# Kernel tuning notes

Measured on AMD Instinct MI355X. Metric: run time of the kernel, lower is better.

Reference implementation:

```python
import jax, jax.numpy as jnp
import numpy as np

B, N, K_NN, H, IN_DIM, OUT_DIM = 32, 1024, 16, 64, 4, 2
START = 2 * H   # EdgeConv MLP input width (cat[x_i, x_j - x_i])
MID = 3 * H // 2


def _elu(x):
    return jax.nn.elu(x)


def _lin_init(key, fan_in, fan_out):
    k1, k2 = jax.random.split(key)
    lim = 1.0 / np.sqrt(fan_in)
    W = jax.random.uniform(k1, (fan_in, fan_out), minval=-lim, maxval=lim, dtype=jnp.float32)
    b = jax.random.uniform(k2, (fan_out,), minval=-lim, maxval=lim, dtype=jnp.float32)
    return W, b


def setup_inputs():
    key = jax.random.key(0)
    ks = jax.random.split(key, 11)
    inp = {
        "x": jax.random.normal(ks[0], (B, N, IN_DIM), dtype=jnp.float32),
        "norm": jnp.array([1e-3, 1e-1, 1.0 / 3.15, 1.0 / 3000.0], dtype=jnp.float32),
    }
    dims = [("in1", IN_DIM, H // 2), ("in2", H // 2, H), ("in3", H, H),
            ("c1a", START, MID), ("c1b", MID, H),
            ("c2a", START, MID), ("c2b", MID, H),
            ("o1", H, H), ("o2", H, H // 2), ("o3", H // 2, OUT_DIM)]
    for i, (nm, fi, fo) in enumerate(dims):
        W, b = _lin_init(ks[i + 1], fi, fo)
        inp[nm + "_W"] = W
        inp[nm + "_b"] = b
    return inp


def _pdist2(x):
    # squared pairwise distances per graph: [B,n,n]
    x2 = jnp.sum(x * x, -1)
    d2 = x2[:, :, None] + x2[:, None, :] - 2.0 * jnp.einsum('bnh,bmh->bnm', x, x)
    return jnp.maximum(d2, 0.0)


def _knn(x, valid, k):
    # knn_graph(loop=False) restricted to valid (non-padded) target columns
    b, n, _ = x.shape
    d2 = _pdist2(jax.lax.stop_gradient(x))
    bad = jnp.eye(n, dtype=bool)[None] | (~valid)[:, None, :]
    d2 = jnp.where(bad, jnp.inf, d2)
    _, idx = jax.lax.top_k(-d2, k)                      # [B,n,k] neighbor ids
    bi = jnp.arange(b)[:, None, None]
    ni = jnp.arange(n)[None, :, None]
    Kd = jnp.zeros((b, n, n), bool).at[bi, ni, idx].set(True)   # dense kNN adjacency
    return idx, Kd


def _edge_mlp(e, W1, b1, W2, b2):
    return _elu(_elu(e @ W1 + b1) @ W2 + b2)


def _edgeconv(x, valid, idx, Kd, W1, b1, W2, b2):
    # EdgeConv(aggr='add') over to_undirected(knn_graph): message nn([x_i, x_j - x_i])
    b, n, h = x.shape
    xj = jax.vmap(lambda xg, ig: xg[ig])(x, idx)        # [B,n,k,h] gathered neighbors
    xi = jnp.broadcast_to(x[:, :, None, :], xj.shape)
    agg = _edge_mlp(jnp.concatenate([xi, xj - xi], -1), W1, b1, W2, b2).sum(2)
    # reverse edges added by to_undirected; coalesce drops duplicates of mutual kNN pairs
    mutual = jnp.take_along_axis(jnp.swapaxes(Kd, 1, 2), idx, axis=2)  # [B,n,k]
    w_rev = ((~mutual) & valid[:, :, None]).astype(x.dtype)
    msg_rev = _edge_mlp(jnp.concatenate([xj, xi - xj], -1), W1, b1, W2, b2) * w_rev[..., None]
    seg = (jnp.arange(b)[:, None, None] * n + idx).reshape(-1)
    agg_rev = jax.ops.segment_sum(msg_rev.reshape(-1, h), seg, num_segments=b * n).reshape(b, n, h)
    return agg + agg_rev


def _norm_cut_w(x, A):
    # normalized_cut_2d: ||x_i - x_j|| * (1/deg_i + 1/deg_j) on edges, -inf elsewhere
    dist = jnp.sqrt(_pdist2(x))
    invdeg = 1.0 / A.sum(-1).astype(x.dtype)
    cut = dist * (invdeg[:, :, None] + invdeg[:, None, :])
    return jnp.where(A, cut, -jnp.inf)


def _graclus(Wm):
    # greedy heavy-edge matching (deterministic node order), like graclus
    n = Wm.shape[-1]

    def match_one(Wg):
        def body(i, st):
            unmatched, cluster = st
            wi = jnp.where(unmatched, Wg[i], -jnp.inf)
            j = jnp.argmax(wi)
            ok = unmatched[i] & jnp.isfinite(wi[j])
            r = jnp.minimum(i, j)
            cluster = jnp.where(ok, cluster.at[i].set(r).at[j].set(r), cluster)
            unmatched = unmatched.at[i].set(False)
            unmatched = jnp.where(ok, unmatched.at[j].set(False), unmatched)
            return unmatched, cluster

        return jax.lax.fori_loop(0, n, body, (jnp.ones(n, bool), jnp.arange(n)))[1]

    return jax.vmap(match_one)(jax.lax.stop_gradient(Wm))


def _max_pool(x, cluster):
    # max over each cluster; representative = min node index; padded slots masked
    b, n, h = x.shape
    pooled = jax.vmap(lambda xg, cg: jax.ops.segment_max(xg, cg, num_segments=n))(x, cluster)
    counts = jax.vmap(lambda cg: jnp.zeros(n, jnp.int32).at[cg].add(1))(cluster)
    valid = counts > 0
    return jnp.where(valid[..., None], pooled, 0.0), valid


def _forward(x, norm, in1_W, in1_b, in2_W, in2_b, in3_W, in3_b,
             c1a_W, c1a_b, c1b_W, c1b_b, c2a_W, c2a_b, c2b_W, c2b_b,
             o1_W, o1_b, o2_W, o2_b, o3_W, o3_b):
    h0 = x * norm
    h0 = _elu(_elu(_elu(h0 @ in1_W + in1_b) @ in2_W + in2_b) @ in3_W + in3_b)
    valid0 = jnp.ones(h0.shape[:2], bool)
    idx1, K1 = _knn(h0, valid0, K_NN)
    h1 = _edgeconv(h0, valid0, idx1, K1, c1a_W, c1a_b, c1b_W, c1b_b)
    A1 = K1 | jnp.swapaxes(K1, 1, 2)
    cl = _graclus(_norm_cut_w(jax.lax.stop_gradient(h1), A1))
    h1p, valid1 = _max_pool(h1, cl)
    idx2, K2 = _knn(h1p, valid1, K_NN)
    h2 = _edgeconv(h1p, valid1, idx2, K2, c2a_W, c2a_b, c2b_W, c2b_b)
    # 2nd graclus max_pool_x followed by global_max_pool == global max over valid nodes
    g = jnp.max(jnp.where(valid1[..., None], h2, -jnp.inf), axis=1)   # [B,H]
    return _elu(_elu(g @ o1_W + o1_b) @ o2_W + o2_b) @ o3_W + o3_b


def reference(x, norm, in1_W, in1_b, in2_W, in2_b, in3_W, in3_b,
              c1a_W, c1a_b, c1b_W, c1b_b, c2a_W, c2a_b, c2b_W, c2b_b,
              o1_W, o1_b, o2_W, o2_b, o3_W, o3_b):
    return _forward(x, norm, in1_W, in1_b, in2_W, in2_b, in3_W, in3_b,
                    c1a_W, c1a_b, c1b_W, c1b_b, c2a_W, c2a_b, c2b_W, c2b_b,
                    o1_W, o1_b, o2_W, o2_b, o3_W, o3_b)
```

## Files before the change

### kernel.cpp

```cpp
#include <hip/hip_runtime.h>
#include <cmath>


#define DEVI __device__ __forceinline__
constexpr int B_   = 32;
constexpr int N_   = 1024;
constexpr int NN   = B_ * N_;
constexpr int NCH  = 8;
constexpr int CHW  = 128;
constexpr int ECAP = 128;

#define INFF (__builtin_huge_valf())

DEVI float elu_(float x)  { return x > 0.f ? x : expm1f(x); }
DEVI float eluf(float x)  { return x > 0.f ? x : __expf(x) - 1.f; }

__global__ __launch_bounds__(256) void k_input(
    const float* __restrict__ x, const float* __restrict__ nrm,
    const float* __restrict__ w1, const float* __restrict__ b1,
    const float* __restrict__ w2, const float* __restrict__ b2,
    const float* __restrict__ w3, const float* __restrict__ b3,
    float* __restrict__ h0, float* __restrict__ x2a)
{
  __shared__ float s1[128], sb1[32], s2[2048], sb2[64], s3[4096], sb3[64];
  int tid = threadIdx.x;
  for (int t = tid; t < 128; t += 256) s1[t] = w1[t];
  if (tid < 32) sb1[tid] = b1[tid];
  for (int t = tid; t < 2048; t += 256) s2[t] = w2[t];
  if (tid < 64) sb2[tid] = b2[tid];
  for (int t = tid; t < 4096; t += 256) s3[t] = w3[t];
  if (tid < 64) sb3[tid] = b3[tid];
  __syncthreads();
  int n = blockIdx.x * 256 + tid;
  float xi[4];
#pragma unroll
  for (int d = 0; d < 4; d++) xi[d] = x[n * 4 + d] * nrm[d];
  float a1[32];
#pragma unroll
  for (int c = 0; c < 32; c++) {
    float a = sb1[c];
#pragma unroll
    for (int d = 0; d < 4; d++) a += xi[d] * s1[d * 32 + c];
    a1[c] = elu_(a);
  }
  float a2[64];
#pragma unroll
  for (int c = 0; c < 64; c++) {
    float a = sb2[c];
#pragma unroll
    for (int d = 0; d < 32; d++) a += a1[d] * s2[d * 64 + c];
    a2[c] = elu_(a);
  }
  float ss = 0.f;
#pragma unroll
  for (int c = 0; c < 64; c++) {
    float a = sb3[c];
#pragma unroll
    for (int d = 0; d < 64; d++) a += a2[d] * s3[d * 64 + c];
    a = elu_(a);
    h0[n * 64 + c] = a;
    ss += a * a;
  }
  x2a[n] = ss;
}

__global__ __launch_bounds__(256) void k_knn(
    const float4* __restrict__ X4, const float* __restrict__ X2,
    const unsigned* __restrict__ vbits, const int* __restrict__ vrows,
    float* __restrict__ pd, unsigned short* __restrict__ pix)
{
  __shared__ float xs[CHW * 64];
  __shared__ float xs2[CHW];
  __shared__ unsigned vm[32];
  int bid = blockIdx.x;
  int swz = (bid & 7) * 128 + (bid >> 3);
  int b  = swz >> 5;
  int rt = (swz >> 3) & 3;
  int ch = swz & 7;
  int tid = threadIdx.x;
  int j0 = ch * CHW;
  for (int t = tid; t < CHW * 16; t += 256) {
    int r = t >> 4, q = t & 15;
    float4 v = X4[(b * N_ + j0 + r) * 16 + q];
    *reinterpret_cast<float4*>(&xs[r * 64 + q * 4]) = v;
  }
  for (int t = tid; t < CHW; t += 256) xs2[t] = X2[b * N_ + j0 + t];
  for (int t = tid; t < 32; t += 256) vm[t] = vbits ? vbits[b * 32 + t] : 0xFFFFFFFFu;
  __syncthreads();
  int i = rt * 256 + tid;
  int gi = b * N_ + i;
  if (vrows && !vrows[gi]) return;
  float4 xi4[16];
#pragma unroll
  for (int q = 0; q < 16; q++) xi4[q] = X4[gi * 16 + q];
  float x2i = X2[gi];
  float topd[16]; int topi[16];
#pragma unroll
  for (int q = 0; q < 16; q++) { topd[q] = INFF; topi[q] = 0xFFFF; }
  for (int jj = 0; jj < CHW; ++jj) {
    int j = j0 + jj;
    if (j == i) continue;
    if (!((vm[j >> 5] >> (j & 31)) & 1u)) continue;
    const float4* xr = reinterpret_cast<const float4*>(&xs[jj * 64]);
    float dot = 0.f;
#pragma unroll
    for (int q = 0; q < 16; q++) {
      float4 v = xr[q];
      dot += xi4[q].x * v.x + xi4[q].y * v.y + xi4[q].z * v.z + xi4[q].w * v.w;
    }
    float d2 = fmaxf(x2i + xs2[jj] - 2.f * dot, 0.f);
    if (d2 < topd[15]) {
      topd[15] = d2; topi[15] = j;
#pragma unroll
      for (int p = 15; p > 0; --p) {
        if (topd[p] < topd[p - 1]) {
          float td = topd[p]; topd[p] = topd[p - 1]; topd[p - 1] = td;
          int   ti = topi[p]; topi[p] = topi[p - 1]; topi[p - 1] = ti;
        }
      }
    }
  }
  size_t base = ((size_t)gi * NCH + ch) * 16;
#pragma unroll
  for (int q = 0; q < 16; q++) { pd[base + q] = topd[q]; pix[base + q] = (unsigned short)topi[q]; }
}

__global__ __launch_bounds__(64) void k_merge(
    const float* __restrict__ pd, const unsigned short* __restrict__ pix,
    const int* __restrict__ vrows,
    unsigned* __restrict__ Kb, unsigned* __restrict__ KTb)
{
  __shared__ unsigned lbm[64][33];
  int tid = threadIdx.x;
  int gi = blockIdx.x * 64 + tid;
  int b = gi >> 10, i = gi & 1023;
  if (vrows && !vrows[gi]) return;
#pragma unroll
  for (int w = 0; w < 32; w++) lbm[tid][w] = 0u;
  float topd[16]; int topi[16];
#pragma unroll
  for (int q = 0; q < 16; q++) { topd[q] = INFF; topi[q] = 0; }
  for (int s = 0; s < NCH; ++s) {
    size_t base = ((size_t)gi * NCH + s) * 16;
#pragma unroll 1
    for (int q = 0; q < 16; q++) {
      float d = pd[base + q];
      if (!(d < topd[15])) break;
      topd[15] = d; topi[15] = pix[base + q];
#pragma unroll
      for (int p = 15; p > 0; --p) {
        if (topd[p] < topd[p - 1]) {
          float td = topd[p]; topd[p] = topd[p - 1]; topd[p - 1] = td;
          int   ti = topi[p]; topi[p] = topi[p - 1]; topi[p - 1] = ti;
        }
      }
    }
  }
#pragma unroll
  for (int q = 0; q < 16; q++) {
    int j = topi[q];
    lbm[tid][j >> 5] |= (1u << (j & 31));
    atomicOr(&KTb[((size_t)b * N_ + j) * 32 + (i >> 5)], 1u << (i & 31));
  }
#pragma unroll
  for (int w = 0; w < 32; w++) Kb[(size_t)gi * 32 + w] = lbm[tid][w];
}

__global__ __launch_bounds__(256) void k_elist(
    const unsigned* __restrict__ Kb, const unsigned* __restrict__ KTb,
    unsigned short* __restrict__ E, int* __restrict__ ecnt, float* __restrict__ invdeg)
{
  int gi = blockIdx.x * 256 + threadIdx.x;
  unsigned short* e = E + (size_t)gi * ECAP;
  int n = 0;
  for (int w = 0; w < 32; w++) {
    unsigned m = Kb[(size_t)gi * 32 + w] | KTb[(size_t)gi * 32 + w];
    while (m) {
      int bit = __ffs(m) - 1; m &= m - 1;
      if (n < ECAP) e[n] = (unsigned short)(w * 32 + bit);
      n++;
    }
  }
  ecnt[gi] = n < ECAP ? n : ECAP;
  if (invdeg) invdeg[gi] = 1.f / (float)n;
}

__global__ __launch_bounds__(256) void k_uv(
    const float* __restrict__ X, const float* __restrict__ W1, const float* __restrict__ b1,
    float* __restrict__ wb, float* __restrict__ vb)
{
  __shared__ float wc[64 * 96], wv[64 * 96];
  int tid = threadIdx.x;
  for (int t = tid; t < 64 * 96; t += 256) {
    int d = t / 96, c = t - d * 96;
    float hv = W1[(d + 64) * 96 + c];
    wv[t] = hv;
    wc[t] = W1[d * 96 + c] - hv;
  }
  __syncthreads();
  int n = blockIdx.x * 256 + tid;
  float xi[64];
#pragma unroll
  for (int q = 0; q < 16; q++) {
    float4 v = reinterpret_cast<const float4*>(X)[n * 16 + q];
    xi[q * 4] = v.x; xi[q * 4 + 1] = v.y; xi[q * 4 + 2] = v.z; xi[q * 4 + 3] = v.w;
  }
#pragma unroll 1
  for (int c4 = 0; c4 < 24; c4++) {
    float aw0 = b1[c4 * 4 + 0], aw1 = b1[c4 * 4 + 1], aw2 = b1[c4 * 4 + 2], aw3 = b1[c4 * 4 + 3];
    float av0 = 0.f, av1 = 0.f, av2 = 0.f, av3 = 0.f;
#pragma unroll
    for (int d = 0; d < 64; d++) {
      float4 c = *reinterpret_cast<const float4*>(&wc[d * 96 + c4 * 4]);
      float4 v = *reinterpret_cast<const float4*>(&wv[d * 96 + c4 * 4]);
      float xd = xi[d];
      aw0 += xd * c.x; aw1 += xd * c.y; aw2 += xd * c.z; aw3 += xd * c.w;
      av0 += xd * v.x; av1 += xd * v.y; av2 += xd * v.z; av3 += xd * v.w;
    }
    wb[(size_t)n * 96 + c4 * 4 + 0] = aw0; wb[(size_t)n * 96 + c4 * 4 + 1] = aw1;
    wb[(size_t)n * 96 + c4 * 4 + 2] = aw2; wb[(size_t)n * 96 + c4 * 4 + 3] = aw3;
    vb[(size_t)n * 96 + c4 * 4 + 0] = av0; vb[(size_t)n * 96 + c4 * 4 + 1] = av1;
    vb[(size_t)n * 96 + c4 * 4 + 2] = av2; vb[(size_t)n * 96 + c4 * 4 + 3] = av3;
  }
}

__global__ __launch_bounds__(256) void k_conv(
    const float* __restrict__ wbuf, const float* __restrict__ vbuf,
    const unsigned short* __restrict__ E, const int* __restrict__ ecnt,
    const int* __restrict__ vrows,
    const float* __restrict__ W2, const float* __restrict__ b2,
    float* __restrict__ out, float* __restrict__ x2out)
{
  __shared__ float w2s[96 * 64];
  __shared__ float b2s[64];
  __shared__ float wds[64 * 100];
  int tid = threadIdx.x;
  int bid = blockIdx.x;
  int swz = (bid & 7) * 64 + (bid >> 3);
  int dst0 = swz * 64;
  for (int t = tid; t < 96 * 64; t += 256) w2s[t] = W2[t];
  if (tid < 64) b2s[tid] = b2[tid];
  for (int t = tid; t < 64 * 96; t += 256) {
    int l = t / 96, c = t - l * 96;
    wds[l * 100 + c] = wbuf[(size_t)(dst0 + l) * 96 + c];
  }
  __syncthreads();
  int dl = tid >> 2, p = tid & 3;
  int dst = dst0 + dl;
  if (vrows && !vrows[dst]) return;
  int cnt = ecnt[dst];
  const unsigned short* e = E + (size_t)dst * ECAP;
  int gb = dst & ~(N_ - 1);
  float agg[16];
#pragma unroll
  for (int o = 0; o < 16; o++) agg[o] = 0.f;

#pragma unroll 1
  for (int k = 0; k < cnt; k += 2) {
    bool hasB = (k + 1 < cnt);
    int sA = gb + e[k];
    int sB = hasB ? gb + e[k + 1] : sA;
    const float4* vA = reinterpret_cast<const float4*>(vbuf + (size_t)sA * 96);
    const float4* vB = reinterpret_cast<const float4*>(vbuf + (size_t)sB * 96);
    float sa[16], sb_[16];
#pragma unroll
    for (int o = 0; o < 16; o++) { sa[o] = b2s[p * 16 + o]; sb_[o] = sa[o]; }
#pragma unroll 1
    for (int c4 = 0; c4 < 24; c4++) {
      float4 wv = *reinterpret_cast<const float4*>(&wds[dl * 100 + c4 * 4]);
      float4 a4 = vA[c4];
      float4 b4 = vB[c4];
      float tA0 = eluf(wv.x + a4.x), tA1 = eluf(wv.y + a4.y),
            tA2 = eluf(wv.z + a4.z), tA3 = eluf(wv.w + a4.w);
      float tB0 = eluf(wv.x + b4.x), tB1 = eluf(wv.y + b4.y),
            tB2 = eluf(wv.z + b4.z), tB3 = eluf(wv.w + b4.w);
      const float* wr = &w2s[(c4 * 4) * 64 + p * 16];
#pragma unroll
      for (int o4 = 0; o4 < 4; o4++) {
        float4 w0 = *reinterpret_cast<const float4*>(wr + 0 * 64 + o4 * 4);
        float4 w1 = *reinterpret_cast<const float4*>(wr + 1 * 64 + o4 * 4);
        float4 w2 = *reinterpret_cast<const float4*>(wr + 2 * 64 + o4 * 4);
        float4 w3 = *reinterpret_cast<const float4*>(wr + 3 * 64 + o4 * 4);
        sa [o4*4+0] += tA0*w0.x + tA1*w1.x + tA2*w2.x + tA3*w3.x;
        sa [o4*4+1] += tA0*w0.y + tA1*w1.y + tA2*w2.y + tA3*w3.y;
        sa [o4*4+2] += tA0*w0.z + tA1*w1.z + tA2*w2.z + tA3*w3.z;
        sa [o4*4+3] += tA0*w0.w + tA1*w1.w + tA2*w2.w + tA3*w3.w;
        sb_[o4*4+0] += tB0*w0.x + tB1*w1.x + tB2*w2.x + tB3*w3.x;
        sb_[o4*4+1] += tB0*w0.y + tB1*w1.y + tB2*w2.y + tB3*w3.y;
        sb_[o4*4+2] += tB0*w0.z + tB1*w1.z + tB2*w2.z + tB3*w3.z;
        sb_[o4*4+3] += tB0*w0.w + tB1*w1.w + tB2*w2.w + tB3*w3.w;
      }
    }
#pragma unroll
    for (int o = 0; o < 16; o++) agg[o] += eluf(sa[o]);
    if (hasB) {
#pragma unroll
      for (int o = 0; o < 16; o++) agg[o] += eluf(sb_[o]);
    }
  }
  float4* o4p = reinterpret_cast<float4*>(out + (size_t)dst * 64 + p * 16);
#pragma unroll
  for (int q = 0; q < 4; q++)
    o4p[q] = make_float4(agg[q*4], agg[q*4+1], agg[q*4+2], agg[q*4+3]);
  if (x2out) {
    float s = 0.f;
#pragma unroll
    for (int o = 0; o < 16; o++) s += agg[o] * agg[o];
    s += __shfl_xor(s, 1, 64);
    s += __shfl_xor(s, 2, 64);
    if (p == 0) x2out[dst] = s;
  }
}

__global__ __launch_bounds__(256) void k_wgt(
    const float* __restrict__ h1, const float* __restrict__ x2h,
    const float* __restrict__ invdeg, const unsigned short* __restrict__ E,
    const int* __restrict__ ecnt, unsigned* __restrict__ cw)
{
  int bid = blockIdx.x;
  int swz = (bid & 7) * 16 + (bid >> 3);
  int gi = swz * 256 + threadIdx.x;
  int base = gi & ~(N_ - 1);
  float xi[64];
#pragma unroll
  for (int q = 0; q < 16; q++) {
    float4 v = reinterpret_cast<const float4*>(h1)[gi * 16 + q];
    xi[q * 4] = v.x; xi[q * 4 + 1] = v.y; xi[q * 4 + 2] = v.z; xi[q * 4 + 3] = v.w;
  }
  float x2i = x2h[gi];
  float idi = invdeg[gi];
  int cnt = ecnt[gi];
  const unsigned short* e = E + (size_t)gi * ECAP;
  unsigned* crow = cw + (size_t)gi * ECAP;
#pragma unroll 1
  for (int n = 0; n < cnt; n++) {
    int j = base + e[n];
    const float4* r = reinterpret_cast<const float4*>(h1 + (size_t)j * 64);
    float dot = 0.f;
#pragma unroll
    for (int q = 0; q < 16; q++) {
      float4 v = r[q];
      dot += xi[q * 4] * v.x + xi[q * 4 + 1] * v.y + xi[q * 4 + 2] * v.z + xi[q * 4 + 3] * v.w;
    }
    float d2 = fmaxf(x2i + x2h[j] - 2.f * dot, 0.f);
    float wgt = sqrtf(d2) * (idi + invdeg[j]);
    crow[n] = __float_as_uint(wgt);
  }
}

__global__ __launch_bounds__(256) void k_sort(
    const unsigned* __restrict__ cw, const unsigned short* __restrict__ E0,
    const int* __restrict__ ecnt, unsigned short* __restrict__ E)
{
  int node = (blockIdx.x * 256 + threadIdx.x) >> 6;
  int lane = threadIdx.x & 63;
  int cnt = ecnt[node];
  size_t rb = (size_t)node * ECAP;
  unsigned long long a = 0ull, b = 0ull;
  if (lane < cnt)
    a = ((unsigned long long)cw[rb + lane] << 32) | (unsigned)(~(unsigned)E0[rb + lane]);
  if (lane + 64 < cnt)
    b = ((unsigned long long)cw[rb + 64 + lane] << 32) | (unsigned)(~(unsigned)E0[rb + 64 + lane]);
#pragma unroll
  for (int k = 2; k <= 128; k <<= 1) {
#pragma unroll
    for (int jj = k >> 1; jj > 0; jj >>= 1) {
      if (jj == 64) {
        unsigned long long mx = a > b ? a : b;
        b = a > b ? b : a;
        a = mx;
      } else {
        unsigned long long oa = __shfl_xor(a, jj, 64);
        bool low   = (lane & jj) == 0;
        bool descA = (lane & k) == 0;
        a = ((low == descA) == (a > oa)) ? a : oa;
        unsigned long long ob = __shfl_xor(b, jj, 64);
        bool descB = (((lane + 64) & k) == 0);
        b = ((low == descB) == (b > ob)) ? b : ob;
      }
    }
  }
  E[rb + lane]      = (unsigned short)(~(unsigned)a);
  E[rb + 64 + lane] = (unsigned short)(~(unsigned)b);
}

__global__ __launch_bounds__(64) void k_graclus(
    const unsigned short* __restrict__ E,
    int* __restrict__ cluster, int* __restrict__ partner)
{
  int b = blockIdx.x, lane = threadIdx.x;
  int g0 = b * N_;
  const unsigned short* Eg = E + (size_t)g0 * ECAP;
  for (int t = lane; t < N_; t += 64) { cluster[g0 + t] = t; partner[g0 + t] = -1; }
  unsigned m16 = 0xFFFFu;
  unsigned long long below = (1ull << lane) - 1ull;

  unsigned short eA0, eA1, eB0, eB1, eC0, eC1, eD0, eD1;
#define LOADROW(E0v, E1v, row)                                                  \
  { size_t rb_ = (size_t)(row) * ECAP;                                          \
    E0v = Eg[rb_ + lane];                                                       \
    E1v = Eg[rb_ + 64 + lane]; }
  LOADROW(eA0, eA1, 0)
  LOADROW(eB0, eB1, 1)
  LOADROW(eC0, eC1, 2)
  LOADROW(eD0, eD1, 3)

  auto step = [&](int i, unsigned short e0, unsigned short e1) {
    unsigned mi = (unsigned)__builtin_amdgcn_readlane((int)m16, i >> 4);
    if ((mi >> (i & 15)) & 1u) {
      bool v0 = e0 != 0xFFFFu, v1 = e1 != 0xFFFFu;
      int j0 = e0 & (N_ - 1), j1 = e1 & (N_ - 1);
      unsigned gm0 = (unsigned)__shfl((int)m16, j0 >> 4, 64);
      unsigned gm1 = (unsigned)__shfl((int)m16, j1 >> 4, 64);
      bool p0 = v0 && ((gm0 >> (j0 & 15)) & 1u);
      bool p1 = v1 && ((gm1 >> (j1 & 15)) & 1u);
      unsigned long long m0 = __ballot(p0);
      unsigned long long m1 = __ballot(p1);
      unsigned long long mm = m0 ? m0 : m1;
      if (mm) {
        int sw = __ffsll((long long)mm) - 1;
        int jw = m0 ? __builtin_amdgcn_readlane(j0, sw)
                    : __builtin_amdgcn_readlane(j1, sw);
        unsigned clr = (lane == (jw >> 4)) ? (1u << (jw & 15)) : 0u;
        m16 &= ~clr;
        if (lane == 0) {
          int r = i < jw ? i : jw;
          int o = i ^ jw ^ r;
          cluster[g0 + o] = r;
          partner[g0 + r] = o;
        }
      }
      unsigned clri = (lane == (i >> 4)) ? (1u << (i & 15)) : 0u;
      m16 &= ~clri;
    }
  };

  for (int i = 0; i < N_; i += 4) {
    step(i, eA0, eA1);
    if (i + 4 < N_) LOADROW(eA0, eA1, i + 4)
    step(i + 1, eB0, eB1);
    if (i + 5 < N_) LOADROW(eB0, eB1, i + 5)
    step(i + 2, eC0, eC1);
    if (i + 6 < N_) LOADROW(eC0, eC1, i + 6)
    step(i + 3, eD0, eD1);
    if (i + 7 < N_) LOADROW(eD0, eD1, i + 7)
  }
#undef LOADROW
}

__global__ __launch_bounds__(256) void k_maxpool(
    const float* __restrict__ h1, const int* __restrict__ cluster, const int* __restrict__ partner,
    float* __restrict__ h1p, float* __restrict__ x2p, int* __restrict__ valid1,
    unsigned* __restrict__ vbits)
{
  int gi = blockIdx.x * 256 + threadIdx.x;
  int b = gi >> 10, i = gi & 1023;
  if (cluster[gi] == i) {
    int p = partner[gi];
    float s = 0.f;
#pragma unroll
    for (int q = 0; q < 16; q++) {
      float4 a = reinterpret_cast<const float4*>(h1)[gi * 16 + q];
      if (p >= 0) {
        float4 c = reinterpret_cast<const float4*>(h1)[(b * N_ + p) * 16 + q];
        a.x = fmaxf(a.x, c.x); a.y = fmaxf(a.y, c.y); a.z = fmaxf(a.z, c.z); a.w = fmaxf(a.w, c.w);
      }
      reinterpret_cast<float4*>(h1p)[gi * 16 + q] = a;
      s += a.x * a.x + a.y * a.y + a.z * a.z + a.w * a.w;
    }
    x2p[gi] = s; valid1[gi] = 1;
    atomicOr(&vbits[b * 32 + (i >> 5)], 1u << (i & 31));
  } else {
    float4 z = make_float4(0.f, 0.f, 0.f, 0.f);
#pragma unroll
    for (int q = 0; q < 16; q++) reinterpret_cast<float4*>(h1p)[gi * 16 + q] = z;
    x2p[gi] = 0.f; valid1[gi] = 0;
  }
}

__global__ __launch_bounds__(256) void k_final(
    const float* __restrict__ h2, const int* __restrict__ valid1,
    const float* __restrict__ o1W, const float* __restrict__ o1b,
    const float* __restrict__ o2W, const float* __restrict__ o2b,
    const float* __restrict__ o3W, const float* __restrict__ o3b,
    float* __restrict__ out)
{
  __shared__ float gm[4][64], g[64], l1[64], l2[32];
  int b = blockIdx.x, tid = threadIdx.x;
  int d = tid & 63, r = tid >> 6;
  float m = -INFF;
  for (int i = r; i < N_; i += 4) {
    if (valid1[b * N_ + i]) m = fmaxf(m, h2[(size_t)(b * N_ + i) * 64 + d]);
  }
  gm[r][d] = m;
  __syncthreads();
  if (tid < 64) g[d] = fmaxf(fmaxf(gm[0][d], gm[1][d]), fmaxf(gm[2][d], gm[3][d]));
  __syncthreads();
  if (tid < 64) {
    float a = o1b[tid];
    for (int c = 0; c < 64; c++) a += g[c] * o1W[c * 64 + tid];
    l1[tid] = elu_(a);
  }
  __syncthreads();
  if (tid < 32) {
    float a2 = o2b[tid];
    for (int c = 0; c < 64; c++) a2 += l1[c] * o2W[c * 32 + tid];
    l2[tid] = elu_(a2);
  }
  __syncthreads();
  if (tid < 2) {
    float a3 = o3b[tid];
    for (int c = 0; c < 32; c++) a3 += l2[c] * o3W[c * 2 + tid];
    out[b * 2 + tid] = a3;
  }
}

extern "C" void kernel_launch(void* const* d_in, const int* in_sizes, int n_in,
                              void* d_out, int out_size, void* d_ws, size_t ws_size,
                              hipStream_t stream)
{
  const float* x    = (const float*)d_in[0];
  const float* nrm  = (const float*)d_in[1];
  const float* in1W = (const float*)d_in[2];  const float* in1b = (const float*)d_in[3];
  const float* in2W = (const float*)d_in[4];  const float* in2b = (const float*)d_in[5];
  const float* in3W = (const float*)d_in[6];  const float* in3b = (const float*)d_in[7];
  const float* c1aW = (const float*)d_in[8];  const float* c1ab = (const float*)d_in[9];
  const float* c1bW = (const float*)d_in[10]; const float* c1bb = (const float*)d_in[11];
  const float* c2aW = (const float*)d_in[12]; const float* c2ab = (const float*)d_in[13];
  const float* c2bW = (const float*)d_in[14]; const float* c2bb = (const float*)d_in[15];
  const float* o1W  = (const float*)d_in[16]; const float* o1b  = (const float*)d_in[17];
  const float* o2W  = (const float*)d_in[18]; const float* o2b  = (const float*)d_in[19];
  const float* o3W  = (const float*)d_in[20]; const float* o3b  = (const float*)d_in[21];

  constexpr size_t O_H0    = 0;
  constexpr size_t O_X2A   = O_H0    + (size_t)NN * 64 * 4;
  constexpr size_t O_U     = O_X2A   + (size_t)NN * 4;
  constexpr size_t O_K     = O_U     + (size_t)NN * NCH * 16 * 6;
  constexpr size_t O_KT    = O_K     + (size_t)NN * 32 * 4;
  constexpr size_t O_H1    = O_KT    + (size_t)NN * 32 * 4;
  constexpr size_t O_X2H   = O_H1    + (size_t)NN * 64 * 4;
  constexpr size_t O_IDG   = O_X2H   + (size_t)NN * 4;
  constexpr size_t O_ECNT  = O_IDG   + (size_t)NN * 4;
  constexpr size_t O_CLU   = O_ECNT  + (size_t)NN * 4;
  constexpr size_t O_PAR   = O_CLU   + (size_t)NN * 4;
  constexpr size_t O_VAL   = O_PAR   + (size_t)NN * 4;
  constexpr size_t O_VBITS = O_VAL   + (size_t)NN * 4;
  constexpr size_t O_E     = O_VBITS + (size_t)B_ * 32 * 4;
  constexpr size_t TOTAL   = O_E     + (size_t)NN * ECAP * 2;
  if (ws_size < TOTAL) return;

  char* w = (char*)d_ws;
  float*          h0   = (float*)(w + O_H0);
  float*          x2a  = (float*)(w + O_X2A);
  float*          pdp  = (float*)(w + O_U);
  unsigned short* pip  = (unsigned short*)(w + O_U + (size_t)NN * NCH * 16 * 4);
  float*          wb   = (float*)(w + O_U);
  float*          vb   = (float*)(w + O_U + (size_t)NN * 96 * 4);
  unsigned*       cwt  = (unsigned*)(w + O_U);
  unsigned*       Kb   = (unsigned*)(w + O_K);
  unsigned*       KTb  = (unsigned*)(w + O_KT);
  float*          h1   = (float*)(w + O_H1);
  float*          x2h  = (float*)(w + O_X2H);
  float*          idg  = (float*)(w + O_IDG);
  int*            ecnt = (int*)(w + O_ECNT);
  int*            clu  = (int*)(w + O_CLU);
  int*            par  = (int*)(w + O_PAR);
  int*            val  = (int*)(w + O_VAL);
  unsigned*       vbits= (unsigned*)(w + O_VBITS);
  unsigned short* E    = (unsigned short*)(w + O_E);
  float* h1p = h0;
  float* x2p = x2a;
  float* h2  = h1;

  k_input<<<NN / 256, 256, 0, stream>>>(x, nrm, in1W, in1b, in2W, in2b, in3W, in3b, h0, x2a);
  k_knn<<<B_ * 32, 256, 0, stream>>>((const float4*)h0, x2a, nullptr, nullptr, pdp, pip);
  hipMemsetAsync(KTb, 0, (size_t)NN * 32 * 4, stream);
  k_merge<<<NN / 64, 64, 0, stream>>>(pdp, pip, nullptr, Kb, KTb);
  k_elist<<<NN / 256, 256, 0, stream>>>(Kb, KTb, E, ecnt, idg);
  k_uv<<<NN / 256, 256, 0, stream>>>(h0, c1aW, c1ab, wb, vb);
  k_conv<<<NN / 64, 256, 0, stream>>>(wb, vb, E, ecnt, nullptr, c1bW, c1bb, h1, x2h);
  k_wgt<<<NN / 256, 256, 0, stream>>>(h1, x2h, idg, E, ecnt, cwt);
  k_sort<<<NN / 4, 256, 0, stream>>>(cwt, E, ecnt, E);
  k_graclus<<<B_, 64, 0, stream>>>(E, clu, par);
  hipMemsetAsync(vbits, 0, (size_t)B_ * 32 * 4, stream);
  k_maxpool<<<NN / 256, 256, 0, stream>>>(h1, clu, par, h1p, x2p, val, vbits);
  k_knn<<<B_ * 32, 256, 0, stream>>>((const float4*)h1p, x2p, vbits, val, pdp, pip);
  hipMemsetAsync(Kb, 0, (size_t)NN * 32 * 4 * 2, stream);
  k_merge<<<NN / 64, 64, 0, stream>>>(pdp, pip, val, Kb, KTb);
  k_elist<<<NN / 256, 256, 0, stream>>>(Kb, KTb, E, ecnt, nullptr);
  k_uv<<<NN / 256, 256, 0, stream>>>(h1p, c2aW, c2ab, wb, vb);
  k_conv<<<NN / 64, 256, 0, stream>>>(wb, vb, E, ecnt, val, c2bW, c2bb, h2, nullptr);
  k_final<<<B_, 256, 0, stream>>>(h2, val, o1W, o1b, o2W, o2b, o3W, o3b, (float*)d_out);
}
```

Before: 1.750 ms.

## Sort EdgeConv destination nodes by degree to balance wavefront work

Adds a per-graph counting-sort kernel that orders nodes by edge count. k_conv then processes destinations through this permutation, so each wavefront handles nodes with similar neighbor-loop trip counts. Each block takes four interleaved degree buckets (low, high, and mirrored) to even out work across blocks. It also drops the early return for invalid rows, since these now cluster in zero-degree groups, and unrolls the inner channel loop by 4. The cost is an extra small kernel launch per conv and gathered, non-contiguous loads of wbuf rows.

```diff
diff --git a/kernel.cpp b/kernel.cpp
--- a/kernel.cpp
+++ b/kernel.cpp
@@ -185,6 +185,28 @@
   if (invdeg) invdeg[gi] = 1.f / (float)n;
 }
 
+__global__ __launch_bounds__(256) void k_perm(
+    const int* __restrict__ ecnt, unsigned short* __restrict__ perm)
+{
+  __shared__ int hist[ECAP + 1];
+  __shared__ int pfx[ECAP + 1];
+  int b = blockIdx.x, tid = threadIdx.x;
+  int g0 = b * N_;
+  for (int t = tid; t <= ECAP; t += 256) hist[t] = 0;
+  __syncthreads();
+  for (int t = tid; t < N_; t += 256) atomicAdd(&hist[ecnt[g0 + t]], 1);
+  __syncthreads();
+  if (tid == 0) {
+    int s = 0;
+    for (int d = 0; d <= ECAP; d++) { pfx[d] = s; s += hist[d]; }
+  }
+  __syncthreads();
+  for (int t = tid; t < N_; t += 256) {
+    int r = atomicAdd(&pfx[ecnt[g0 + t]], 1);
+    perm[g0 + r] = (unsigned short)t;
+  }
+}
+
 __global__ __launch_bounds__(256) void k_uv(
     const float* __restrict__ X, const float* __restrict__ W1, const float* __restrict__ b1,
     float* __restrict__ wb, float* __restrict__ vb)
@@ -227,30 +249,36 @@
 __global__ __launch_bounds__(256) void k_conv(
     const float* __restrict__ wbuf, const float* __restrict__ vbuf,
     const unsigned short* __restrict__ E, const int* __restrict__ ecnt,
-    const int* __restrict__ vrows,
+    const unsigned short* __restrict__ perm,
     const float* __restrict__ W2, const float* __restrict__ b2,
     float* __restrict__ out, float* __restrict__ x2out)
 {
   __shared__ float w2s[96 * 64];
   __shared__ float b2s[64];
   __shared__ float wds[64 * 100];
+  __shared__ unsigned short dstl[64];
   int tid = threadIdx.x;
   int bid = blockIdx.x;
   int swz = (bid & 7) * 64 + (bid >> 3);
-  int dst0 = swz * 64;
+  int g  = swz >> 4, kk = swz & 15;
+  int gb = g * N_;
   for (int t = tid; t < 96 * 64; t += 256) w2s[t] = W2[t];
   if (tid < 64) b2s[tid] = b2[tid];
+  if (tid < 64) {
+    int w = tid >> 4, r = tid & 15;
+    int wg = (w == 0) ? kk : (w == 1) ? 31 - kk : (w == 2) ? 32 + kk : 63 - kk;
+    dstl[tid] = perm[gb + wg * 16 + r];
+  }
+  __syncthreads();
   for (int t = tid; t < 64 * 96; t += 256) {
     int l = t / 96, c = t - l * 96;
-    wds[l * 100 + c] = wbuf[(size_t)(dst0 + l) * 96 + c];
+    wds[l * 100 + c] = wbuf[(size_t)(gb + dstl[l]) * 96 + c];
   }
   __syncthreads();
   int dl = tid >> 2, p = tid & 3;
-  int dst = dst0 + dl;
-  if (vrows && !vrows[dst]) return;
+  int dst = gb + dstl[dl];
   int cnt = ecnt[dst];
   const unsigned short* e = E + (size_t)dst * ECAP;
-  int gb = dst & ~(N_ - 1);
   float agg[16];
 #pragma unroll
   for (int o = 0; o < 16; o++) agg[o] = 0.f;
@@ -265,7 +293,7 @@
     float sa[16], sb_[16];
 #pragma unroll
     for (int o = 0; o < 16; o++) { sa[o] = b2s[p * 16 + o]; sb_[o] = sa[o]; }
-#pragma unroll 1
+#pragma unroll 4
     for (int c4 = 0; c4 < 24; c4++) {
       float4 wv = *reinterpret_cast<const float4*>(&wds[dl * 100 + c4 * 4]);
       float4 a4 = vA[c4];
@@ -546,7 +574,8 @@
   constexpr size_t O_VAL   = O_PAR   + (size_t)NN * 4;
   constexpr size_t O_VBITS = O_VAL   + (size_t)NN * 4;
   constexpr size_t O_E     = O_VBITS + (size_t)B_ * 32 * 4;
-  constexpr size_t TOTAL   = O_E     + (size_t)NN * ECAP * 2;
+  constexpr size_t O_PERM  = O_E     + (size_t)NN * ECAP * 2;
+  constexpr size_t TOTAL   = O_PERM  + (size_t)NN * 2;
   if (ws_size < TOTAL) return;
 
   char* w = (char*)d_ws;
@@ -568,6 +597,7 @@
   int*            val  = (int*)(w + O_VAL);
   unsigned*       vbits= (unsigned*)(w + O_VBITS);
   unsigned short* E    = (unsigned short*)(w + O_E);
+  unsigned short* perm = (unsigned short*)(w + O_PERM);
   float* h1p = h0;
   float* x2p = x2a;
   float* h2  = h1;
@@ -577,8 +607,9 @@
   hipMemsetAsync(KTb, 0, (size_t)NN * 32 * 4, stream);
   k_merge<<<NN / 64, 64, 0, stream>>>(pdp, pip, nullptr, Kb, KTb);
   k_elist<<<NN / 256, 256, 0, stream>>>(Kb, KTb, E, ecnt, idg);
+  k_perm<<<B_, 256, 0, stream>>>(ecnt, perm);
   k_uv<<<NN / 256, 256, 0, stream>>>(h0, c1aW, c1ab, wb, vb);
-  k_conv<<<NN / 64, 256, 0, stream>>>(wb, vb, E, ecnt, nullptr, c1bW, c1bb, h1, x2h);
+  k_conv<<<NN / 64, 256, 0, stream>>>(wb, vb, E, ecnt, perm, c1bW, c1bb, h1, x2h);
   k_wgt<<<NN / 256, 256, 0, stream>>>(h1, x2h, idg, E, ecnt, cwt);
   k_sort<<<NN / 4, 256, 0, stream>>>(cwt, E, ecnt, E);
   k_graclus<<<B_, 64, 0, stream>>>(E, clu, par);
@@ -588,7 +619,8 @@
   hipMemsetAsync(Kb, 0, (size_t)NN * 32 * 4 * 2, stream);
   k_merge<<<NN / 64, 64, 0, stream>>>(pdp, pip, val, Kb, KTb);
   k_elist<<<NN / 256, 256, 0, stream>>>(Kb, KTb, E, ecnt, nullptr);
+  k_perm<<<B_, 256, 0, stream>>>(ecnt, perm);
   k_uv<<<NN / 256, 256, 0, stream>>>(h1p, c2aW, c2ab, wb, vb);
-  k_conv<<<NN / 64, 256, 0, stream>>>(wb, vb, E, ecnt, val, c2bW, c2bb, h2, nullptr);
+  k_conv<<<NN / 64, 256, 0, stream>>>(wb, vb, E, ecnt, perm, c2bW, c2bb, h2, nullptr);
   k_final<<<B_, 256, 0, stream>>>(h2, val, o1W, o1b, o2W, o2b, o3W, o3b, (float*)d_out);
 }
```

Result: faster. 1.628 ms (-7.0%).
